# Kernel tuning notes

Measured on AMD Instinct MI355X. Metric: run time of the kernel, lower is better.

Reference implementation:

```python
import jax, jax.numpy as jnp
import numpy as np

N, F_IN, N_CLASSES = 8192, 512, 345


def setup_inputs() -> dict:
    key = jax.random.key(0)
    k = jax.random.split(key, 5)
    x = jax.random.normal(k[0], (N, F_IN), dtype=jnp.float32)
    adj = jax.random.uniform(k[1], (N, N), dtype=jnp.float32)
    # scale like a row-normalized adjacency so activations stay sane
    adj = adj / jnp.sum(adj, axis=1, keepdims=True)
    W1 = jax.random.normal(k[2], (F_IN, F_IN), dtype=jnp.float32) * (1.0 / np.sqrt(F_IN))
    b1 = jnp.zeros((F_IN,), dtype=jnp.float32)
    W2 = jax.random.normal(k[3], (F_IN, N_CLASSES), dtype=jnp.float32) * (1.0 / np.sqrt(F_IN))
    b2 = jnp.zeros((N_CLASSES,), dtype=jnp.float32)
    return {"x": x, "adj": adj, "W1": W1, "b1": b1, "W2": W2, "b2": b2}


def reference(x, adj, W1, b1, W2, b2):
    # GraphConvolution: out = adj @ (x @ W) + b  (Kipf GCN layer, dense adj)
    h = jnp.maximum(adj @ (x @ W1) + b1, 0.0)  # relu(conv_1(x, adj))
    # dropout is identity in eval mode (deterministic reference)
    logit = adj @ (h @ W2) + b2                # classifier(h, adj)
    return logit
```

## Files before the change

kernel.cpp:

```cpp
#include <hip/hip_runtime.h>
#include <cstdint>
#include <cstddef>


#define NN 8192
#define FIN 512
#define NCLS 345
#define NCLS_PAD 384

typedef __attribute__((ext_vector_type(8))) short bf16x8;
typedef __attribute__((ext_vector_type(4))) float f32x4;

__device__ __forceinline__ unsigned short f2bf(float f) {
  unsigned u = __float_as_uint(f);
  u += 0x7fffu + ((u >> 16) & 1u);
  return (unsigned short)(u >> 16);
}

__global__ void tconv_kernel(const float* __restrict__ in, unsigned short* __restrict__ out,
                             int K, int Nin, int Npad) {
  __shared__ float t[32][33];
  int kb = blockIdx.x * 32, nb = blockIdx.y * 32;
  int x = threadIdx.x, y = threadIdx.y;
#pragma unroll
  for (int i = 0; i < 32; i += 8) {
    int k = kb + y + i, n = nb + x;
    t[y + i][x] = (n < Nin) ? in[(size_t)k * Nin + n] : 0.0f;
  }
  __syncthreads();
#pragma unroll
  for (int i = 0; i < 32; i += 8) {
    int n = nb + y + i, k = kb + x;
    out[(size_t)n * K + k] = f2bf(t[x][y + i]);
  }
}

__global__ void conv_adj_kernel(const float* __restrict__ in, unsigned short* __restrict__ out) {
  size_t i = ((size_t)blockIdx.x * 256 + threadIdx.x) * 4;
  float4 v = *(const float4*)(in + i);
  ushort4 w;
  w.x = f2bf(v.x); w.y = f2bf(v.y); w.z = f2bf(v.z); w.w = f2bf(v.w);
  *(ushort4*)(out + i) = w;
}

template <bool ABF, int OMODE, bool BIAS, bool RELU>
__global__ __launch_bounds__(256, 1) void gemm_kernel(
    const void* __restrict__ Ap, const unsigned short* __restrict__ Bt,
    const float* __restrict__ bias, void* __restrict__ Cp,
    const int M, const int N, const int K, const int ldc, const int nbound) {
  __shared__ __align__(16) char smem[32768];

  const int tid = threadIdx.x;
  const int lane = tid & 63, wave = tid >> 6;
  const int wr = wave >> 1, wc = wave & 1;
  const int ln15 = lane & 15, lhi = lane >> 4;

  const int gn = N >> 7;
  int bid = blockIdx.x;
  {
    const int q = (int)gridDim.x >> 3;
    bid = (bid & 7) * q + (bid >> 3);
  }
  const int bm = (bid / gn) << 7;
  const int bn = (bid % gn) << 7;

  const int sm = tid >> 1;
  const int sk = (tid & 1) << 5;
  const int wxor = (sm & 7) << 4;
  const int wbaseA = sm * 128;
  const int wbaseB = 16384 + sm * 128;

  const float* Af = (const float*)Ap;
  const unsigned short* Ab = (const unsigned short*)Ap;
  const size_t arow = (size_t)(bm + sm) * K + sk;
  const unsigned short* Bsrc = Bt + (size_t)(bn + sm) * K + sk;

  int a_base[2], b_base[2];
#pragma unroll
  for (int kh = 0; kh < 2; kh++) {
    int kb = ((kh << 5) + (lhi << 3)) << 1;
    int kx = kb ^ ((ln15 & 7) << 4);
    a_base[kh] = (wr * 64 + ln15) * 128 + kx;
    b_base[kh] = 16384 + (wc * 64 + ln15) * 128 + kx;
  }

  f32x4 acc[4][4];
#pragma unroll
  for (int i = 0; i < 4; i++)
#pragma unroll
    for (int j = 0; j < 4; j++) acc[i][j] = (f32x4)(0.0f);

  float4 pf[8];
  bf16x8 pa[4];
  bf16x8 pb[4];

  auto load_A = [&](int k0) {
    if constexpr (ABF) {
      const unsigned short* s = Ab + arow + k0;
#pragma unroll
      for (int j = 0; j < 4; j++) pa[j] = *(const bf16x8*)(s + 8 * j);
    } else {
      const float* s = Af + arow + k0;
#pragma unroll
      for (int j = 0; j < 8; j++) pf[j] = *(const float4*)(s + 4 * j);
    }
  };
  auto load_B = [&](int k0) {
    const unsigned short* s = Bsrc + k0;
#pragma unroll
    for (int j = 0; j < 4; j++) pb[j] = *(const bf16x8*)(s + 8 * j);
  };

  load_A(0);
  load_B(0);

  for (int k0 = 0; k0 < K; k0 += 64) {
    __syncthreads();
    if constexpr (ABF) {
#pragma unroll
      for (int j = 0; j < 4; j++) {
        int off = wbaseA + ((sk * 2 + 16 * j) ^ wxor);
        *(bf16x8*)(smem + off) = pa[j];
      }
    } else {
#pragma unroll
      for (int j = 0; j < 8; j++) {
        ushort4 v;
        v.x = f2bf(pf[j].x); v.y = f2bf(pf[j].y);
        v.z = f2bf(pf[j].z); v.w = f2bf(pf[j].w);
        int off = wbaseA + (((sk + 4 * j) * 2) ^ wxor);
        *(ushort4*)(smem + off) = v;
      }
    }
#pragma unroll
    for (int j = 0; j < 4; j++) {
      int off = wbaseB + ((sk * 2 + 16 * j) ^ wxor);
      *(bf16x8*)(smem + off) = pb[j];
    }
    __syncthreads();

    int kn = k0 + 64;
    if (kn >= K) kn = 0;
    load_A(kn);
    load_B(kn);

#pragma unroll
    for (int kh = 0; kh < 2; kh++) {
      bf16x8 afr[4], bfr[4];
#pragma unroll
      for (int mi = 0; mi < 4; mi++)
        afr[mi] = *(const bf16x8*)(smem + a_base[kh] + mi * 2048);
#pragma unroll
      for (int ni = 0; ni < 4; ni++)
        bfr[ni] = *(const bf16x8*)(smem + b_base[kh] + ni * 2048);
#pragma unroll
      for (int mi = 0; mi < 4; mi++)
#pragma unroll
        for (int ni = 0; ni < 4; ni++)
          acc[mi][ni] = __builtin_amdgcn_mfma_f32_16x16x32_bf16(
              afr[mi], bfr[ni], acc[mi][ni], 0, 0, 0);
    }
  }

  if constexpr (OMODE == 2) {
    unsigned short* Ct = (unsigned short*)Cp;
#pragma unroll
    for (int ni = 0; ni < 4; ni++) {
      int n = bn + wc * 64 + ni * 16 + ln15;
#pragma unroll
      for (int mi = 0; mi < 4; mi++) {
        int m0 = bm + wr * 64 + mi * 16 + (lhi << 2);
        ushort4 v;
        v.x = f2bf(acc[mi][ni][0]); v.y = f2bf(acc[mi][ni][1]);
        v.z = f2bf(acc[mi][ni][2]); v.w = f2bf(acc[mi][ni][3]);
        *(ushort4*)(Ct + (size_t)n * ldc + m0) = v;
      }
    }
  } else if constexpr (OMODE == 1) {
    unsigned short* Ch = (unsigned short*)Cp;
#pragma unroll
    for (int ni = 0; ni < 4; ni++) {
      int n = bn + wc * 64 + ni * 16 + ln15;
      float bv = BIAS ? bias[n] : 0.0f;
#pragma unroll
      for (int mi = 0; mi < 4; mi++) {
        int m0 = bm + wr * 64 + mi * 16 + (lhi << 2);
#pragma unroll
        for (int r = 0; r < 4; r++) {
          float v = acc[mi][ni][r] + bv;
          if (RELU) v = fmaxf(v, 0.0f);
          Ch[(size_t)(m0 + r) * ldc + n] = f2bf(v);
        }
      }
    }
  } else {
    float* Cf = (float*)Cp;
#pragma unroll
    for (int ni = 0; ni < 4; ni++) {
      int n = bn + wc * 64 + ni * 16 + ln15;
      if (n < nbound) {
        float bv = BIAS ? bias[n] : 0.0f;
#pragma unroll
        for (int mi = 0; mi < 4; mi++) {
          int m0 = bm + wr * 64 + mi * 16 + (lhi << 2);
#pragma unroll
          for (int r = 0; r < 4; r++) {
            float v = acc[mi][ni][r] + bv;
            if (RELU) v = fmaxf(v, 0.0f);
            Cf[(size_t)(m0 + r) * ldc + n] = v;
          }
        }
      }
    }
  }
}

extern "C" void kernel_launch(void* const* d_in, const int* in_sizes, int n_in,
                              void* d_out, int out_size, void* d_ws, size_t ws_size,
                              hipStream_t stream) {
  (void)in_sizes; (void)n_in; (void)out_size;
  const float* x   = (const float*)d_in[0];
  const float* adj = (const float*)d_in[1];
  const float* W1  = (const float*)d_in[2];
  const float* b1  = (const float*)d_in[3];
  const float* W2  = (const float*)d_in[4];
  const float* b2  = (const float*)d_in[5];

  char* w = (char*)d_ws;
  size_t off = 0;
  auto alloc = [&](size_t bytes) -> char* {
    char* p = w + off;
    off += (bytes + 255) & ~(size_t)255;
    return p;
  };
  unsigned short* W1T   = (unsigned short*)alloc((size_t)FIN * FIN * 2);
  unsigned short* W2T   = (unsigned short*)alloc((size_t)NCLS_PAD * FIN * 2);
  unsigned short* tmp1T = (unsigned short*)alloc((size_t)FIN * NN * 2);
  unsigned short* hbuf  = (unsigned short*)alloc((size_t)NN * FIN * 2);
  unsigned short* tmp2T = (unsigned short*)alloc((size_t)NCLS_PAD * NN * 2);
  const size_t adj_bytes = (size_t)NN * NN * 2;
  const bool big = (off + adj_bytes) <= ws_size;
  unsigned short* adjb = big ? (unsigned short*)alloc(adj_bytes) : nullptr;

  dim3 blk(256);

  tconv_kernel<<<dim3(FIN / 32, FIN / 32), dim3(32, 8), 0, stream>>>(W1, W1T, FIN, FIN, FIN);
  tconv_kernel<<<dim3(FIN / 32, NCLS_PAD / 32), dim3(32, 8), 0, stream>>>(W2, W2T, FIN, NCLS, NCLS_PAD);
  if (big)
    conv_adj_kernel<<<dim3((NN * (size_t)NN) / (256 * 4)), blk, 0, stream>>>(adj, adjb);

  gemm_kernel<false, 2, false, false><<<dim3(64 * 4), blk, 0, stream>>>(
      x, W1T, nullptr, tmp1T, NN, FIN, FIN, NN, FIN);
  if (big)
    gemm_kernel<true, 1, true, true><<<dim3(64 * 4), blk, 0, stream>>>(
        adjb, tmp1T, b1, hbuf, NN, FIN, NN, FIN, FIN);
  else
    gemm_kernel<false, 1, true, true><<<dim3(64 * 4), blk, 0, stream>>>(
        adj, tmp1T, b1, hbuf, NN, FIN, NN, FIN, FIN);
  gemm_kernel<true, 2, false, false><<<dim3(64 * 3), blk, 0, stream>>>(
      hbuf, W2T, nullptr, tmp2T, NN, NCLS_PAD, FIN, NN, NCLS_PAD);
  if (big)
    gemm_kernel<true, 0, true, false><<<dim3(64 * 3), blk, 0, stream>>>(
        adjb, tmp2T, b2, d_out, NN, NCLS_PAD, NN, NCLS, NCLS);
  else
    gemm_kernel<false, 0, true, false><<<dim3(64 * 3), blk, 0, stream>>>(
        adj, tmp2T, b2, d_out, NN, NCLS_PAD, NN, NCLS, NCLS);
}
```

Before: 760.6 us.

## Add split-K GEMMs with fp32 partial buffers and reduction kernels

Each GEMM is now split along K (2-way for the small feature transforms, 4-way for the adjacency products). Partial fp32 tiles go to a workspace buffer, and new reduce kernels sum them, then apply bias, ReLU, bf16 conversion or transpose. The goal is more workgroups to fill the 256 CUs, which were underused with only 192–256 tiles. Launch bounds also rise to allow 4 blocks per CU. The cost is extra partial-sum traffic (up to 64MB written and read back per big GEMM), extra launches, and a larger workspace requirement.

```diff
diff --git a/kernel.cpp b/kernel.cpp
--- a/kernel.cpp
+++ b/kernel.cpp
@@ -43,8 +43,68 @@
   *(ushort4*)(out + i) = w;
 }
 
-template <bool ABF, int OMODE, bool BIAS, bool RELU>
-__global__ __launch_bounds__(256, 1) void gemm_kernel(
+__global__ void reduce_elem2(const float* __restrict__ P, unsigned short* __restrict__ out,
+                             size_t total) {
+  size_t i = ((size_t)blockIdx.x * 256 + threadIdx.x) * 4;
+  float4 a = *(const float4*)(P + i);
+  float4 b = *(const float4*)(P + total + i);
+  ushort4 o;
+  o.x = f2bf(a.x + b.x); o.y = f2bf(a.y + b.y);
+  o.z = f2bf(a.z + b.z); o.w = f2bf(a.w + b.w);
+  *(ushort4*)(out + i) = o;
+}
+
+template <int KS, bool RELU, bool OUTF32>
+__global__ void reduce_trans(const float* __restrict__ P, const float* __restrict__ bias,
+                             void* __restrict__ out, const int M, const int NW,
+                             const int nbound, const int ldo) {
+  __shared__ float t[64][65];
+  const int tm = blockIdx.x, tn = blockIdx.y;
+  const int tid = threadIdx.x;
+  const int nl = tid >> 4, m4 = (tid & 15) << 2;
+  const size_t SS = (size_t)NW * M;
+#pragma unroll
+  for (int p = 0; p < 4; p++) {
+    int nr = p * 16 + nl;
+    const float* src = P + (size_t)(tn * 64 + nr) * M + tm * 64 + m4;
+    float4 s = *(const float4*)src;
+#pragma unroll
+    for (int ksl = 1; ksl < KS; ksl++) {
+      float4 v = *(const float4*)(src + (size_t)ksl * SS);
+      s.x += v.x; s.y += v.y; s.z += v.z; s.w += v.w;
+    }
+    t[nr][m4 + 0] = s.x; t[nr][m4 + 1] = s.y;
+    t[nr][m4 + 2] = s.z; t[nr][m4 + 3] = s.w;
+  }
+  __syncthreads();
+#pragma unroll
+  for (int p = 0; p < 4; p++) {
+    int ml = p * 16 + (tid >> 4);
+    int n0 = (tid & 15) << 2;
+    int m = tm * 64 + ml;
+    int ng = tn * 64 + n0;
+    float v[4];
+#pragma unroll
+    for (int j = 0; j < 4; j++) {
+      float bv = (ng + j < nbound) ? bias[ng + j] : 0.0f;
+      v[j] = t[n0 + j][ml] + bv;
+      if (RELU) v[j] = fmaxf(v[j], 0.0f);
+    }
+    if (OUTF32) {
+      float* of = (float*)out;
+#pragma unroll
+      for (int j = 0; j < 4; j++)
+        if (ng + j < nbound) of[(size_t)m * ldo + ng + j] = v[j];
+    } else {
+      ushort4 o;
+      o.x = f2bf(v[0]); o.y = f2bf(v[1]); o.z = f2bf(v[2]); o.w = f2bf(v[3]);
+      *(ushort4*)((unsigned short*)out + (size_t)m * ldo + ng) = o;
+    }
+  }
+}
+
+template <bool ABF, int OMODE, bool BIAS, bool RELU, int KS>
+__global__ __launch_bounds__(256, 4) void gemm_kernel(
     const void* __restrict__ Ap, const unsigned short* __restrict__ Bt,
     const float* __restrict__ bias, void* __restrict__ Cp,
     const int M, const int N, const int K, const int ldc, const int nbound) {
@@ -55,14 +115,25 @@
   const int wr = wave >> 1, wc = wave & 1;
   const int ln15 = lane & 15, lhi = lane >> 4;
 
-  const int gn = N >> 7;
   int bid = blockIdx.x;
   {
     const int q = (int)gridDim.x >> 3;
     bid = (bid & 7) * q + (bid >> 3);
   }
-  const int bm = (bid / gn) << 7;
-  const int bn = (bid % gn) << 7;
+  const int gn = N >> 7;
+  int bmi, bnid, ks;
+  if constexpr (KS == 1) {
+    bmi = bid / gn; bnid = bid % gn; ks = 0;
+  } else {
+    bnid = bid % gn;
+    int t = bid / gn;
+    ks = t % KS; bmi = t / KS;
+  }
+  const int bm = bmi << 7;
+  const int bn = bnid << 7;
+  const int Kc = K / KS;
+  const int kbeg = ks * Kc;
+  const int kend = kbeg + Kc;
 
   const int sm = tid >> 1;
   const int sk = (tid & 1) << 5;
@@ -111,10 +182,10 @@
     for (int j = 0; j < 4; j++) pb[j] = *(const bf16x8*)(s + 8 * j);
   };
 
-  load_A(0);
-  load_B(0);
-
-  for (int k0 = 0; k0 < K; k0 += 64) {
+  load_A(kbeg);
+  load_B(kbeg);
+
+  for (int k0 = kbeg; k0 < kend; k0 += 64) {
     __syncthreads();
     if constexpr (ABF) {
 #pragma unroll
@@ -140,7 +211,7 @@
     __syncthreads();
 
     int kn = k0 + 64;
-    if (kn >= K) kn = 0;
+    if (kn >= kend) kn = kbeg;
     load_A(kn);
     load_B(kn);
 
@@ -162,7 +233,18 @@
     }
   }
 
-  if constexpr (OMODE == 2) {
+  if constexpr (OMODE == 4) {
+    float* P = (float*)Cp + (size_t)ks * N * M;
+#pragma unroll
+    for (int ni = 0; ni < 4; ni++) {
+      int n = bn + wc * 64 + ni * 16 + ln15;
+#pragma unroll
+      for (int mi = 0; mi < 4; mi++) {
+        int m0 = bm + wr * 64 + mi * 16 + (lhi << 2);
+        *(f32x4*)(P + (size_t)n * M + m0) = acc[mi][ni];
+      }
+    }
+  } else if constexpr (OMODE == 2) {
     unsigned short* Ct = (unsigned short*)Cp;
 #pragma unroll
     for (int ni = 0; ni < 4; ni++) {
@@ -238,9 +320,15 @@
   unsigned short* tmp1T = (unsigned short*)alloc((size_t)FIN * NN * 2);
   unsigned short* hbuf  = (unsigned short*)alloc((size_t)NN * FIN * 2);
   unsigned short* tmp2T = (unsigned short*)alloc((size_t)NCLS_PAD * NN * 2);
-  const size_t adj_bytes = (size_t)NN * NN * 2;
-  const bool big = (off + adj_bytes) <= ws_size;
-  unsigned short* adjb = big ? (unsigned short*)alloc(adj_bytes) : nullptr;
+
+  const size_t P_BYTES = (size_t)4 * FIN * NN * 4;
+  const size_t ADJ_BYTES = (size_t)NN * NN * 2;
+  float* Pbuf = nullptr;
+  unsigned short* adjb = nullptr;
+  if (off + P_BYTES <= ws_size) Pbuf = (float*)alloc(P_BYTES);
+  if (off + ADJ_BYTES <= ws_size) adjb = (unsigned short*)alloc(ADJ_BYTES);
+  const bool sk = (Pbuf != nullptr);
+  const bool big = (adjb != nullptr);
 
   dim3 blk(256);
 
@@ -249,20 +337,59 @@
   if (big)
     conv_adj_kernel<<<dim3((NN * (size_t)NN) / (256 * 4)), blk, 0, stream>>>(adj, adjb);
 
-  gemm_kernel<false, 2, false, false><<<dim3(64 * 4), blk, 0, stream>>>(
-      x, W1T, nullptr, tmp1T, NN, FIN, FIN, NN, FIN);
-  if (big)
-    gemm_kernel<true, 1, true, true><<<dim3(64 * 4), blk, 0, stream>>>(
-        adjb, tmp1T, b1, hbuf, NN, FIN, NN, FIN, FIN);
-  else
-    gemm_kernel<false, 1, true, true><<<dim3(64 * 4), blk, 0, stream>>>(
-        adj, tmp1T, b1, hbuf, NN, FIN, NN, FIN, FIN);
-  gemm_kernel<true, 2, false, false><<<dim3(64 * 3), blk, 0, stream>>>(
-      hbuf, W2T, nullptr, tmp2T, NN, NCLS_PAD, FIN, NN, NCLS_PAD);
-  if (big)
-    gemm_kernel<true, 0, true, false><<<dim3(64 * 3), blk, 0, stream>>>(
-        adjb, tmp2T, b2, d_out, NN, NCLS_PAD, NN, NCLS, NCLS);
-  else
-    gemm_kernel<false, 0, true, false><<<dim3(64 * 3), blk, 0, stream>>>(
-        adj, tmp2T, b2, d_out, NN, NCLS_PAD, NN, NCLS, NCLS);
-}
+  if (sk) {
+    gemm_kernel<false, 4, false, false, 2><<<dim3(64 * 4 * 2), blk, 0, stream>>>(
+        x, W1T, nullptr, Pbuf, NN, FIN, FIN, 0, 0);
+    reduce_elem2<<<dim3((FIN * (size_t)NN) / 1024), blk, 0, stream>>>(
+        Pbuf, tmp1T, (size_t)FIN * NN);
+  } else {
+    gemm_kernel<false, 2, false, false, 1><<<dim3(64 * 4), blk, 0, stream>>>(
+        x, W1T, nullptr, tmp1T, NN, FIN, FIN, NN, FIN);
+  }
+
+  if (sk) {
+    if (big)
+      gemm_kernel<true, 4, false, false, 4><<<dim3(64 * 4 * 4), blk, 0, stream>>>(
+          adjb, tmp1T, nullptr, Pbuf, NN, FIN, NN, 0, 0);
+    else
+      gemm_kernel<false, 4, false, false, 4><<<dim3(64 * 4 * 4), blk, 0, stream>>>(
+          adj, tmp1T, nullptr, Pbuf, NN, FIN, NN, 0, 0);
+    reduce_trans<4, true, false><<<dim3(NN / 64, FIN / 64), blk, 0, stream>>>(
+        Pbuf, b1, hbuf, NN, FIN, FIN, FIN);
+  } else {
+    if (big)
+      gemm_kernel<true, 1, true, true, 1><<<dim3(64 * 4), blk, 0, stream>>>(
+          adjb, tmp1T, b1, hbuf, NN, FIN, NN, FIN, FIN);
+    else
+      gemm_kernel<false, 1, true, true, 1><<<dim3(64 * 4), blk, 0, stream>>>(
+          adj, tmp1T, b1, hbuf, NN, FIN, NN, FIN, FIN);
+  }
+
+  if (sk) {
+    gemm_kernel<true, 4, false, false, 2><<<dim3(64 * 3 * 2), blk, 0, stream>>>(
+        hbuf, W2T, nullptr, Pbuf, NN, NCLS_PAD, FIN, 0, 0);
+    reduce_elem2<<<dim3((NCLS_PAD * (size_t)NN) / 1024), blk, 0, stream>>>(
+        Pbuf, tmp2T, (size_t)NCLS_PAD * NN);
+  } else {
+    gemm_kernel<true, 2, false, false, 1><<<dim3(64 * 3), blk, 0, stream>>>(
+        hbuf, W2T, nullptr, tmp2T, NN, NCLS_PAD, FIN, NN, NCLS_PAD);
+  }
+
+  if (sk) {
+    if (big)
+      gemm_kernel<true, 4, false, false, 4><<<dim3(64 * 3 * 4), blk, 0, stream>>>(
+          adjb, tmp2T, nullptr, Pbuf, NN, NCLS_PAD, NN, 0, 0);
+    else
+      gemm_kernel<false, 4, false, false, 4><<<dim3(64 * 3 * 4), blk, 0, stream>>>(
+          adj, tmp2T, nullptr, Pbuf, NN, NCLS_PAD, NN, 0, 0);
+    reduce_trans<4, false, true><<<dim3(NN / 64, NCLS_PAD / 64), blk, 0, stream>>>(
+        Pbuf, b2, d_out, NN, NCLS_PAD, NCLS, NCLS);
+  } else {
+    if (big)
+      gemm_kernel<true, 0, true, false, 1><<<dim3(64 * 3), blk, 0, stream>>>(
+          adjb, tmp2T, b2, d_out, NN, NCLS_PAD, NN, NCLS, NCLS);
+    else
+      gemm_kernel<false, 0, true, false, 1><<<dim3(64 * 3), blk, 0, stream>>>(
+          adj, tmp2T, b2, d_out, NN, NCLS_PAD, NN, NCLS, NCLS);
+  }
+}
```

After: 650.6 us. -14.5%, faster.
